# Kernel optimization log

Hardware: AMD Instinct MI355X
Metric: run time of the kernel (lower is better)

Reference implementation:

```python
import jax, jax.numpy as jnp
import numpy as np

B, L, D, E, N, DDELTA, DCONV = 4, 2048, 1024, 2048, 16, 64, 4
EPS = 1e-5


def setup_inputs() -> dict:
    key = jax.random.key(0)
    ks = jax.random.split(key, 12)
    def rn(k, shape, scale=0.02):
        return (jax.random.normal(k, shape) * scale).astype(jnp.float32)
    return {
        "resid":  jax.random.normal(ks[0], (B, L, D), dtype=jnp.float32),
        "norm_w": jnp.ones((D,), jnp.float32),
        "skip_w": rn(ks[1], (E, D)),          # skip_proj.weight
        "in_w":   rn(ks[2], (E, D)),          # in_proj.weight
        "conv_w": rn(ks[3], (E, 1, DCONV), 0.1),  # depthwise conv1d weight
        "conv_b": jnp.zeros((E,), jnp.float32),
        "Wd1":    rn(ks[4], (DDELTA, E)),     # W_delta_1.weight
        "Wd2_w":  rn(ks[5], (E, DDELTA)),     # W_delta_2.weight
        "Wd2_b":  rn(ks[6], (E,), 0.01),      # W_delta_2.bias
        "WB":     rn(ks[7], (N, E)),          # W_B.weight
        "WC":     rn(ks[8], (N, E)),          # W_C.weight
        "A_log":  (jax.random.normal(ks[9], (E, N)) * 0.5).astype(jnp.float32),
        "W_D":    jnp.ones((E,), jnp.float32),
        "out_w":  rn(ks[10], (D, E)),         # out_proj.weight
    }


def reference(resid, norm_w, skip_w, in_w, conv_w, conv_b, Wd1, Wd2_w, Wd2_b,
              WB, WC, A_log, W_D, out_w):
    # RMSNorm
    x = resid * jax.lax.rsqrt(jnp.mean(resid * resid, axis=-1, keepdims=True) + EPS) * norm_w
    skip = x @ skip_w.T                              # [B,L,E]
    x = x @ in_w.T                                   # [B,L,E]
    # depthwise causal conv1d (padding=DCONV-1 then truncate to L == left-pad only)
    xc = jnp.transpose(x, (0, 2, 1))                 # [B,E,L]
    xc = jax.lax.conv_general_dilated(
        xc, conv_w, window_strides=(1,), padding=[(DCONV - 1, 0)],
        dimension_numbers=("NCH", "OIH", "NCH"), feature_group_count=conv_w.shape[0])
    x = jnp.transpose(xc, (0, 2, 1)) + conv_b        # [B,L,E]
    x = jax.nn.silu(x)                               # ssm input

    A = -jnp.exp(A_log)                              # [E,N]
    delta = jax.nn.softplus((x @ Wd1.T) @ Wd2_w.T + Wd2_b)  # [B,L,E]
    Bm = x @ WB.T                                    # [B,L,N]
    Cm = x @ WC.T                                    # [B,L,N]

    def step(h, inp):
        x_l, d_l, B_l, C_l = inp                     # [B,E],[B,E],[B,N],[B,N]
        A_bar = jnp.exp(d_l[:, :, None] * A)         # [B,E,N]
        h = A_bar * h + (d_l * x_l)[:, :, None] * B_l[:, None, :]
        y_l = jnp.einsum("ben,bn->be", h, C_l)       # h @ C
        return h, y_l

    h0 = jnp.zeros((resid.shape[0], A.shape[0], A.shape[1]), x.dtype)
    xs = (jnp.swapaxes(x, 0, 1), jnp.swapaxes(delta, 0, 1),
          jnp.swapaxes(Bm, 0, 1), jnp.swapaxes(Cm, 0, 1))
    _, ys = jax.lax.scan(step, h0, xs)               # ys: [L,B,E]
    y = jnp.swapaxes(ys, 0, 1)                       # [B,L,E]

    y = y + x * W_D
    y = y * jax.nn.silu(skip)
    y = y @ out_w.T                                  # [B,L,D]
    return resid + y
```

## Files before the change

kernel.cpp:

```cpp
#include <hip/hip_runtime.h>
#include <hip/hip_bf16.h>
#include <math.h>

#define B_ 4
#define L_ 2048
#define D_ 1024
#define E_ 2048
#define N_ 16
#define DD_ 64
#define DCONV_ 4

#define S_SEG 8
#define SEGLEN_ (L_ / S_SEG)
#define CL_ 32

typedef __attribute__((ext_vector_type(8))) short bf16x8;
typedef __attribute__((ext_vector_type(4))) float f32x4;

static __device__ __forceinline__ float silu_f(float x) {
    return x / (1.f + __expf(-x));
}

static __device__ __forceinline__ ushort f2bf(float f) {
    __hip_bfloat16 h = __float2bfloat16(f);
    return *reinterpret_cast<ushort*>(&h);
}

__global__ __launch_bounds__(256) void k_rmsnorm_bf(const float* __restrict__ resid,
                                                    const float* __restrict__ nw,
                                                    ushort* __restrict__ out) {
    int row = blockIdx.x;
    const float* r = resid + (size_t)row * D_;
    int t = threadIdx.x;
    float4 v = *reinterpret_cast<const float4*>(&r[t * 4]);
    float ss = v.x * v.x + v.y * v.y + v.z * v.z + v.w * v.w;
#pragma unroll
    for (int o = 32; o >= 1; o >>= 1) ss += __shfl_xor(ss, o, 64);
    __shared__ float red[4];
    if ((t & 63) == 0) red[t >> 6] = ss;
    __syncthreads();
    float tot = red[0] + red[1] + red[2] + red[3];
    float rs = rsqrtf(tot * (1.f / (float)D_) + 1e-5f);
    float4 w4 = *reinterpret_cast<const float4*>(&nw[t * 4]);
    ushort4 o4;
    o4.x = f2bf(v.x * rs * w4.x);
    o4.y = f2bf(v.y * rs * w4.y);
    o4.z = f2bf(v.z * rs * w4.z);
    o4.w = f2bf(v.w * rs * w4.w);
    *reinterpret_cast<ushort4*>(&out[(size_t)row * D_ + t * 4]) = o4;
}

__global__ __launch_bounds__(256) void k_cast_bf(const float* __restrict__ in,
                                                 ushort* __restrict__ out) {
    int i = blockIdx.x * 256 + threadIdx.x;
    float4 v = *reinterpret_cast<const float4*>(&in[i * 4]);
    ushort4 o;
    o.x = f2bf(v.x); o.y = f2bf(v.y); o.z = f2bf(v.z); o.w = f2bf(v.w);
    *reinterpret_cast<ushort4*>(&out[i * 4]) = o;
}

template <int EPI>
__global__ __launch_bounds__(256) void k_gemm_bf(const ushort* __restrict__ A,
                                                 const ushort* __restrict__ W,
                                                 const float* __restrict__ addsrc,
                                                 float* __restrict__ C,
                                                 int M, int N, int K) {
    constexpr int BM = 128, BN = 128, BK = 32, LDB = 40;
    __shared__ __align__(16) ushort As[BM * LDB];
    __shared__ __align__(16) ushort Ws[BN * LDB];
    int t = threadIdx.x;
    int m0 = blockIdx.y * BM, n0 = blockIdx.x * BN;
    int wave = t >> 6, lane = t & 63;
    int wr = wave >> 1, wc = wave & 1;
    int lr = lane & 15, lg = lane >> 4;

    f32x4 acc[4][4] = {};

    for (int k0 = 0; k0 < K; k0 += BK) {
#pragma unroll
        for (int p = 0; p < 2; ++p) {
            int f = t + p * 256;
            int row = f >> 2;
            int cg = (f & 3) * 8;
            *reinterpret_cast<uint4*>(&As[row * LDB + cg]) =
                *reinterpret_cast<const uint4*>(&A[(size_t)(m0 + row) * K + k0 + cg]);
            *reinterpret_cast<uint4*>(&Ws[row * LDB + cg]) =
                *reinterpret_cast<const uint4*>(&W[(size_t)(n0 + row) * K + k0 + cg]);
        }
        __syncthreads();
        bf16x8 af[4], bfr[4];
#pragma unroll
        for (int i = 0; i < 4; ++i) {
            af[i]  = *reinterpret_cast<const bf16x8*>(&As[(wr * 64 + i * 16 + lr) * LDB + lg * 8]);
            bfr[i] = *reinterpret_cast<const bf16x8*>(&Ws[(wc * 64 + i * 16 + lr) * LDB + lg * 8]);
        }
#pragma unroll
        for (int i = 0; i < 4; ++i)
#pragma unroll
            for (int j = 0; j < 4; ++j)
                acc[i][j] = __builtin_amdgcn_mfma_f32_16x16x32_bf16(af[i], bfr[j], acc[i][j], 0, 0, 0);
        __syncthreads();
    }

#pragma unroll
    for (int i = 0; i < 4; ++i) {
        int mrow = m0 + wr * 64 + i * 16 + lg * 4;
#pragma unroll
        for (int j = 0; j < 4; ++j) {
            int ncol = n0 + wc * 64 + j * 16 + lr;
#pragma unroll
            for (int q = 0; q < 4; ++q) {
                float v = acc[i][j][q];
                size_t idx = (size_t)(mrow + q) * N + ncol;
                if (EPI == 2) v += addsrc[idx];
                C[idx] = v;
            }
        }
    }
}

__global__ __launch_bounds__(256) void k_proj(const ushort* __restrict__ A,
                                              const ushort* __restrict__ Wc,
                                              float* __restrict__ Bm,
                                              float* __restrict__ Cm,
                                              float* __restrict__ d1) {
    constexpr int BK = 32, LDB = 40;
    __shared__ __align__(16) ushort As[32 * LDB];
    __shared__ __align__(16) ushort Ws[96 * LDB];
    int t = threadIdx.x;
    int m0 = blockIdx.x * 32;
    int wave = t >> 6, lane = t & 63;
    int rowbase = (wave >> 1) * 16;
    int colbase = (wave & 1) * 48;
    int lr = lane & 15, lg = lane >> 4;

    f32x4 acc[3] = {};

    for (int k0 = 0; k0 < E_; k0 += BK) {
        if (t < 128) {
            int row = t >> 2;
            int cg = (t & 3) * 8;
            *reinterpret_cast<uint4*>(&As[row * LDB + cg]) =
                *reinterpret_cast<const uint4*>(&A[(size_t)(m0 + row) * E_ + k0 + cg]);
        }
        {
            int f = t;
            int row = f >> 2, cg = (f & 3) * 8;
            *reinterpret_cast<uint4*>(&Ws[row * LDB + cg]) =
                *reinterpret_cast<const uint4*>(&Wc[(size_t)row * E_ + k0 + cg]);
            if (t < 128) {
                int f2 = t + 256;
                int row2 = f2 >> 2, cg2 = (f2 & 3) * 8;
                *reinterpret_cast<uint4*>(&Ws[row2 * LDB + cg2]) =
                    *reinterpret_cast<const uint4*>(&Wc[(size_t)row2 * E_ + k0 + cg2]);
            }
        }
        __syncthreads();
        bf16x8 af = *reinterpret_cast<const bf16x8*>(&As[(rowbase + lr) * LDB + lg * 8]);
#pragma unroll
        for (int j = 0; j < 3; ++j) {
            bf16x8 bf = *reinterpret_cast<const bf16x8*>(&Ws[(colbase + j * 16 + lr) * LDB + lg * 8]);
            acc[j] = __builtin_amdgcn_mfma_f32_16x16x32_bf16(af, bf, acc[j], 0, 0, 0);
        }
        __syncthreads();
    }

#pragma unroll
    for (int j = 0; j < 3; ++j) {
        int ncol = colbase + j * 16 + lr;
#pragma unroll
        for (int q = 0; q < 4; ++q) {
            int m = m0 + rowbase + lg * 4 + q;
            float v = acc[j][q];
            if (ncol < 16)      Bm[(size_t)m * 16 + ncol] = v;
            else if (ncol < 32) Cm[(size_t)m * 16 + (ncol - 16)] = v;
            else                d1[(size_t)m * 64 + (ncol - 32)] = v;
        }
    }
}

template <int EPI>
__global__ __launch_bounds__(256) void k_gemm_tn(const float* __restrict__ A,
                                                 const float* __restrict__ W,
                                                 const float* __restrict__ bias,
                                                 float* __restrict__ C,
                                                 int M, int N, int K) {
    constexpr int BM = 64, BN = 64, BK = 32;
    constexpr int LDP = 68;
    __shared__ __align__(16) float As[BK][LDP];
    __shared__ __align__(16) float Ws[BK][LDP];
    int tid = threadIdx.x;
    int tx = tid & 15;
    int ty = tid >> 4;
    int m0 = blockIdx.y * BM;
    int n0 = blockIdx.x * BN;

    float acc[4][4];
#pragma unroll
    for (int i = 0; i < 4; ++i)
#pragma unroll
        for (int j = 0; j < 4; ++j) acc[i][j] = 0.f;

    for (int k0 = 0; k0 < K; k0 += BK) {
#pragma unroll
        for (int p = 0; p < 2; ++p) {
            int idx = tid + p * 256;
            int row = idx >> 3;
            int col4 = (idx & 7) * 4;
            float4 av = *reinterpret_cast<const float4*>(&A[(size_t)(m0 + row) * K + k0 + col4]);
            As[col4 + 0][row] = av.x;
            As[col4 + 1][row] = av.y;
            As[col4 + 2][row] = av.z;
            As[col4 + 3][row] = av.w;
            float4 wv = *reinterpret_cast<const float4*>(&W[(size_t)(n0 + row) * K + k0 + col4]);
            Ws[col4 + 0][row] = wv.x;
            Ws[col4 + 1][row] = wv.y;
            Ws[col4 + 2][row] = wv.z;
            Ws[col4 + 3][row] = wv.w;
        }
        __syncthreads();
#pragma unroll
        for (int kk = 0; kk < BK; ++kk) {
            float4 a4 = *reinterpret_cast<const float4*>(&As[kk][ty * 4]);
            float4 b4 = *reinterpret_cast<const float4*>(&Ws[kk][tx * 4]);
            float a[4] = {a4.x, a4.y, a4.z, a4.w};
            float b[4] = {b4.x, b4.y, b4.z, b4.w};
#pragma unroll
            for (int i = 0; i < 4; ++i)
#pragma unroll
                for (int j = 0; j < 4; ++j) acc[i][j] = fmaf(a[i], b[j], acc[i][j]);
        }
        __syncthreads();
    }

#pragma unroll
    for (int i = 0; i < 4; ++i) {
        int m = m0 + ty * 4 + i;
        int nbase = n0 + tx * 4;
        float4 o4;
        float vals[4];
#pragma unroll
        for (int j = 0; j < 4; ++j) {
            float v = acc[i][j];
            if (EPI == 1) {
                float z = v + bias[nbase + j];
                vals[j] = (z > 20.f) ? z : log1pf(expf(z));
            } else {
                vals[j] = v;
            }
        }
        o4.x = vals[0]; o4.y = vals[1]; o4.z = vals[2]; o4.w = vals[3];
        *reinterpret_cast<float4*>(&C[(size_t)m * N + nbase]) = o4;
    }
}

__global__ __launch_bounds__(256) void k_conv_silu(const float* __restrict__ x,
                                                   const float* __restrict__ w,
                                                   const float* __restrict__ bias,
                                                   float* __restrict__ out,
                                                   ushort* __restrict__ out_bf) {
    int idx = blockIdx.x * 256 + threadIdx.x;
    int e = idx & (E_ - 1);
    int l = (idx / E_) & (L_ - 1);
    float4 wv = *reinterpret_cast<const float4*>(&w[e * 4]);
    float acc = bias[e];
    acc = fmaf(wv.w, x[idx], acc);
    if (l >= 1) acc = fmaf(wv.z, x[idx - E_], acc);
    if (l >= 2) acc = fmaf(wv.y, x[idx - 2 * E_], acc);
    if (l >= 3) acc = fmaf(wv.x, x[idx - 3 * E_], acc);
    float s = silu_f(acc);
    out[idx] = s;
    out_bf[idx] = f2bf(s);
}

__global__ __launch_bounds__(256) void k_scan_p1(const float* __restrict__ xs,
                                                 const float* __restrict__ delta,
                                                 const float* __restrict__ Bm,
                                                 const float* __restrict__ A_log,
                                                 float* __restrict__ hloc,
                                                 float* __restrict__ sdsum) {
    __shared__ __align__(16) float sd[CL_][64];
    __shared__ __align__(16) float sx[CL_][64];
    __shared__ __align__(16) float sB[CL_][16];
    int t = threadIdx.x;
    int q = t & 3, ci = t >> 2;
    int bid = blockIdx.x;
    int s = bid & 7;
    int eblk = (bid >> 3) & 31;
    int b = bid >> 8;
    int e0 = eblk * 64;
    int e = e0 + ci;

    f32x4 A4;
    {
        f32x4 al = *reinterpret_cast<const f32x4*>(&A_log[e * 16 + q * 4]);
#pragma unroll
        for (int i = 0; i < 4; ++i) A4[i] = -__expf(al[i]);
    }
    f32x4 h = {0.f, 0.f, 0.f, 0.f};
    float sdl = 0.f;

    for (int l0 = 0; l0 < SEGLEN_; l0 += CL_) {
        size_t rowbase = (size_t)b * L_ + s * SEGLEN_ + l0;
#pragma unroll
        for (int p = 0; p < 2; ++p) {
            int f = t + p * 256;
            int l = f >> 4;
            int c4 = (f & 15) * 4;
            size_t g = (rowbase + l) * E_ + e0 + c4;
            *reinterpret_cast<f32x4*>(&sd[l][c4]) = *reinterpret_cast<const f32x4*>(&delta[g]);
            *reinterpret_cast<f32x4*>(&sx[l][c4]) = *reinterpret_cast<const f32x4*>(&xs[g]);
        }
        if (t < 128) {
            int l = t >> 2;
            int c4 = (t & 3) * 4;
            *reinterpret_cast<f32x4*>(&sB[l][c4]) =
                *reinterpret_cast<const f32x4*>(&Bm[(rowbase + l) * 16 + c4]);
        }
        __syncthreads();
#pragma unroll 4
        for (int l = 0; l < CL_; ++l) {
            float d = sd[l][ci];
            float xv = sx[l][ci];
            f32x4 Bv = *reinterpret_cast<const f32x4*>(&sB[l][q * 4]);
            f32x4 e4;
#pragma unroll
            for (int i = 0; i < 4; ++i) e4[i] = __expf(d * A4[i]);
            float dx = d * xv;
            h = e4 * h + dx * Bv;
            sdl += d;
        }
        __syncthreads();
    }
    size_t idx = (size_t)(b * S_SEG + s) * E_ + e;
    *reinterpret_cast<f32x4*>(&hloc[idx * 16 + q * 4]) = h;
    if (q == 0) sdsum[idx] = sdl;
}

__global__ __launch_bounds__(256) void k_scan_p2(const float* __restrict__ hloc,
                                                 const float* __restrict__ sdsum,
                                                 const float* __restrict__ A_log,
                                                 float* __restrict__ hin) {
    int t = blockIdx.x * 256 + threadIdx.x;
    int q = t & 3;
    int e = (t >> 2) & (E_ - 1);
    int b = t >> 13;
    f32x4 A4;
    {
        f32x4 al = *reinterpret_cast<const f32x4*>(&A_log[e * 16 + q * 4]);
#pragma unroll
        for (int i = 0; i < 4; ++i) A4[i] = -__expf(al[i]);
    }
    f32x4 acc = {0.f, 0.f, 0.f, 0.f};
#pragma unroll
    for (int s = 0; s < S_SEG; ++s) {
        size_t idx = (size_t)(b * S_SEG + s) * E_ + e;
        *reinterpret_cast<f32x4*>(&hin[idx * 16 + q * 4]) = acc;
        float sd = sdsum[idx];
        f32x4 hl = *reinterpret_cast<const f32x4*>(&hloc[idx * 16 + q * 4]);
        f32x4 p;
#pragma unroll
        for (int i = 0; i < 4; ++i) p[i] = __expf(A4[i] * sd);
        acc = hl + p * acc;
    }
}

__global__ __launch_bounds__(256) void k_scan_p3(const float* __restrict__ xs,
                                                 const float* __restrict__ delta,
                                                 const float* __restrict__ Bm,
                                                 const float* __restrict__ Cm,
                                                 const float* __restrict__ A_log,
                                                 const float* __restrict__ W_D,
                                                 const float* __restrict__ skip,
                                                 const float* __restrict__ hin,
                                                 ushort* __restrict__ yg) {
    __shared__ __align__(16) float sd[CL_][64];
    __shared__ __align__(16) float sx[CL_][64];
    __shared__ __align__(16) float ssk[CL_][64];
    __shared__ __align__(16) float sB[CL_][16];
    __shared__ __align__(16) float sC[CL_][16];
    __shared__ __align__(16) ushort syg[CL_][64];
    int t = threadIdx.x;
    int q = t & 3, ci = t >> 2;
    int bid = blockIdx.x;
    int s = bid & 7;
    int eblk = (bid >> 3) & 31;
    int b = bid >> 8;
    int e0 = eblk * 64;
    int e = e0 + ci;

    f32x4 A4;
    {
        f32x4 al = *reinterpret_cast<const f32x4*>(&A_log[e * 16 + q * 4]);
#pragma unroll
        for (int i = 0; i < 4; ++i) A4[i] = -__expf(al[i]);
    }
    size_t cidx = (size_t)(b * S_SEG + s) * E_ + e;
    f32x4 h = *reinterpret_cast<const f32x4*>(&hin[cidx * 16 + q * 4]);
    float wd = W_D[e];

    for (int l0 = 0; l0 < SEGLEN_; l0 += CL_) {
        size_t rowbase = (size_t)b * L_ + s * SEGLEN_ + l0;
#pragma unroll
        for (int p = 0; p < 2; ++p) {
            int f = t + p * 256;
            int l = f >> 4;
            int c4 = (f & 15) * 4;
            size_t g = (rowbase + l) * E_ + e0 + c4;
            *reinterpret_cast<f32x4*>(&sd[l][c4])  = *reinterpret_cast<const f32x4*>(&delta[g]);
            *reinterpret_cast<f32x4*>(&sx[l][c4])  = *reinterpret_cast<const f32x4*>(&xs[g]);
            *reinterpret_cast<f32x4*>(&ssk[l][c4]) = *reinterpret_cast<const f32x4*>(&skip[g]);
        }
        {
            int f = t & 127;
            int l = f >> 2;
            int c4 = (f & 3) * 4;
            size_t gb = (rowbase + l) * 16 + c4;
            if (t < 128)
                *reinterpret_cast<f32x4*>(&sB[l][c4]) = *reinterpret_cast<const f32x4*>(&Bm[gb]);
            else
                *reinterpret_cast<f32x4*>(&sC[l][c4]) = *reinterpret_cast<const f32x4*>(&Cm[gb]);
        }
        __syncthreads();
#pragma unroll 4
        for (int l = 0; l < CL_; ++l) {
            float d = sd[l][ci];
            float xv = sx[l][ci];
            f32x4 Bv = *reinterpret_cast<const f32x4*>(&sB[l][q * 4]);
            f32x4 Cv = *reinterpret_cast<const f32x4*>(&sC[l][q * 4]);
            f32x4 e4;
#pragma unroll
            for (int i = 0; i < 4; ++i) e4[i] = __expf(d * A4[i]);
            float dx = d * xv;
            h = e4 * h + dx * Bv;
            f32x4 yp = h * Cv;
            float y = (yp[0] + yp[1]) + (yp[2] + yp[3]);
            y += __shfl_xor(y, 1, 64);
            y += __shfl_xor(y, 2, 64);
            if (q == 0) {
                float g = silu_f(ssk[l][ci]);
                syg[l][ci] = f2bf((y + xv * wd) * g);
            }
        }
        __syncthreads();
        {
            int l = t >> 3;
            int col = (t & 7) * 8;
            *reinterpret_cast<uint4*>(&yg[(rowbase + l) * E_ + e0 + col]) =
                *reinterpret_cast<const uint4*>(&syg[l][col]);
        }
    }
}

extern "C" void kernel_launch(void* const* d_in, const int* in_sizes, int n_in,
                              void* d_out, int out_size, void* d_ws, size_t ws_size,
                              hipStream_t stream) {
    const float* resid  = (const float*)d_in[0];
    const float* norm_w = (const float*)d_in[1];
    const float* skip_w = (const float*)d_in[2];
    const float* in_w   = (const float*)d_in[3];
    const float* conv_w = (const float*)d_in[4];
    const float* conv_b = (const float*)d_in[5];
    const float* Wd1    = (const float*)d_in[6];
    const float* Wd2_w  = (const float*)d_in[7];
    const float* Wd2_b  = (const float*)d_in[8];
    const float* WB     = (const float*)d_in[9];
    const float* WC     = (const float*)d_in[10];
    const float* A_log  = (const float*)d_in[11];
    const float* W_D    = (const float*)d_in[12];
    const float* out_w  = (const float*)d_in[13];
    float* out = (float*)d_out;

    const int M = B_ * L_;
    char* p = (char*)d_ws;
    ushort* xn_bf   = (ushort*)p;  p += (size_t)M * D_ * 2;
    ushort* skw_bf  = (ushort*)p;  p += (size_t)E_ * D_ * 2;
    ushort* inw_bf  = (ushort*)p;  p += (size_t)E_ * D_ * 2;
    ushort* outw_bf = (ushort*)p;  p += (size_t)D_ * E_ * 2;
    ushort* yg_bf   = (ushort*)p;  p += (size_t)M * E_ * 2;
    float*  skipb   = (float*)p;   p += (size_t)M * E_ * 4;
    float*  xin     = (float*)p;   p += (size_t)M * E_ * 4;
    float*  xs      = (float*)p;   p += (size_t)M * E_ * 4;
    float*  d1      = (float*)p;   p += (size_t)M * DD_ * 4;
    float*  Bm      = (float*)p;   p += (size_t)M * 16 * 4;
    float*  Cm      = (float*)p;   p += (size_t)M * 16 * 4;
    ushort* wbc_bf  = (ushort*)p;  p += (size_t)96 * E_ * 2;
    float*  delta   = xin;
    ushort* xs_bf   = yg_bf;
    float*  hloc    = (float*)xn_bf;
    float*  hin     = hloc + (size_t)B_ * S_SEG * E_ * 16;
    float*  sdsum   = hin  + (size_t)B_ * S_SEG * E_ * 16;

    dim3 blk(256);

    k_cast_bf<<<dim3((E_ * D_) / 1024), blk, 0, stream>>>(skip_w, skw_bf);
    k_cast_bf<<<dim3((E_ * D_) / 1024), blk, 0, stream>>>(in_w, inw_bf);
    k_cast_bf<<<dim3((D_ * E_) / 1024), blk, 0, stream>>>(out_w, outw_bf);
    k_cast_bf<<<dim3((N_ * E_) / 1024), blk, 0, stream>>>(WB, wbc_bf);
    k_cast_bf<<<dim3((N_ * E_) / 1024), blk, 0, stream>>>(WC, wbc_bf + (size_t)16 * E_);
    k_cast_bf<<<dim3((DD_ * E_) / 1024), blk, 0, stream>>>(Wd1, wbc_bf + (size_t)32 * E_);
    k_rmsnorm_bf<<<dim3(M), blk, 0, stream>>>(resid, norm_w, xn_bf);
    k_gemm_bf<0><<<dim3(E_ / 128, M / 128), blk, 0, stream>>>(xn_bf, skw_bf, nullptr, skipb, M, E_, D_);
    k_gemm_bf<0><<<dim3(E_ / 128, M / 128), blk, 0, stream>>>(xn_bf, inw_bf, nullptr, xin, M, E_, D_);
    k_conv_silu<<<dim3((M * E_) / 256), blk, 0, stream>>>(xin, conv_w, conv_b, xs, xs_bf);
    k_proj<<<dim3(M / 32), blk, 0, stream>>>(xs_bf, wbc_bf, Bm, Cm, d1);
    k_gemm_tn<1><<<dim3(E_ / 64, M / 64), blk, 0, stream>>>(d1, Wd2_w, Wd2_b, delta, M, E_, DD_);
    k_scan_p1<<<dim3(B_ * 32 * S_SEG), blk, 0, stream>>>(xs, delta, Bm, A_log, hloc, sdsum);
    k_scan_p2<<<dim3((B_ * E_ * 4) / 256), blk, 0, stream>>>(hloc, sdsum, A_log, hin);
    k_scan_p3<<<dim3(B_ * 32 * S_SEG), blk, 0, stream>>>(xs, delta, Bm, Cm, A_log, W_D,
                                                          skipb, hin, yg_bf);
    k_gemm_bf<2><<<dim3(D_ / 128, M / 128), blk, 0, stream>>>(yg_bf, outw_bf, resid, out, M, D_, E_);
}
```

Before: 664.9 us.

## Restructure scan to one-thread-per-channel, async LDS GEMM loads, bf16 MFMA delta projection

The chunked scan drops its LDS staging and 4-thread-per-channel layout. Each thread now owns one channel with all 16 states in registers, across 32 segments instead of 8, and uses exp2f with pre-scaled A. The bf16 GEMM loads tiles with global_load_lds direct-to-LDS into an unpadded layout. The fp32 SIMT delta GEMM is replaced by the bf16 MFMA GEMM with a fused softplus epilogue, and d1 is now stored as bf16. Risks include LDS bank conflicts from removing the padding, reduced precision in delta, and more register pressure in the scan.

```diff
diff --git a/kernel.cpp b/kernel.cpp
--- a/kernel.cpp
+++ b/kernel.cpp
@@ -10,12 +10,14 @@
 #define DD_ 64
 #define DCONV_ 4
 
-#define S_SEG 8
+#define S_SEG 32
 #define SEGLEN_ (L_ / S_SEG)
-#define CL_ 32
 
 typedef __attribute__((ext_vector_type(8))) short bf16x8;
 typedef __attribute__((ext_vector_type(4))) float f32x4;
+
+typedef __attribute__((address_space(1))) const void gvoid_t;
+typedef __attribute__((address_space(3))) void lvoid_t;
 
 static __device__ __forceinline__ float silu_f(float x) {
     return x / (1.f + __expf(-x));
@@ -25,6 +27,8 @@
     __hip_bfloat16 h = __float2bfloat16(f);
     return *reinterpret_cast<ushort*>(&h);
 }
+
+#define LOG2E_ 1.4426950408889634f
 
 __global__ __launch_bounds__(256) void k_rmsnorm_bf(const float* __restrict__ resid,
                                                     const float* __restrict__ nw,
@@ -62,37 +66,41 @@
 template <int EPI>
 __global__ __launch_bounds__(256) void k_gemm_bf(const ushort* __restrict__ A,
                                                  const ushort* __restrict__ W,
+                                                 const float* __restrict__ bias,
                                                  const float* __restrict__ addsrc,
                                                  float* __restrict__ C,
                                                  int M, int N, int K) {
-    constexpr int BM = 128, BN = 128, BK = 32, LDB = 40;
-    __shared__ __align__(16) ushort As[BM * LDB];
-    __shared__ __align__(16) ushort Ws[BN * LDB];
+    constexpr int BM = 128, BN = 128, BK = 32;
+    __shared__ __align__(16) ushort As[BM * BK];
+    __shared__ __align__(16) ushort Ws[BN * BK];
     int t = threadIdx.x;
     int m0 = blockIdx.y * BM, n0 = blockIdx.x * BN;
     int wave = t >> 6, lane = t & 63;
     int wr = wave >> 1, wc = wave & 1;
     int lr = lane & 15, lg = lane >> 4;
+    int srow = lane >> 2;
+    int scol = (lane & 3) * 8;
 
     f32x4 acc[4][4] = {};
 
     for (int k0 = 0; k0 < K; k0 += BK) {
 #pragma unroll
         for (int p = 0; p < 2; ++p) {
-            int f = t + p * 256;
-            int row = f >> 2;
-            int cg = (f & 3) * 8;
-            *reinterpret_cast<uint4*>(&As[row * LDB + cg]) =
-                *reinterpret_cast<const uint4*>(&A[(size_t)(m0 + row) * K + k0 + cg]);
-            *reinterpret_cast<uint4*>(&Ws[row * LDB + cg]) =
-                *reinterpret_cast<const uint4*>(&W[(size_t)(n0 + row) * K + k0 + cg]);
+            int seg = wave * 2 + p;
+            int row = seg * 16 + srow;
+            __builtin_amdgcn_global_load_lds(
+                (gvoid_t*)(A + (size_t)(m0 + row) * K + k0 + scol),
+                (lvoid_t*)(As + seg * 512), 16, 0, 0);
+            __builtin_amdgcn_global_load_lds(
+                (gvoid_t*)(W + (size_t)(n0 + row) * K + k0 + scol),
+                (lvoid_t*)(Ws + seg * 512), 16, 0, 0);
         }
         __syncthreads();
         bf16x8 af[4], bfr[4];
 #pragma unroll
         for (int i = 0; i < 4; ++i) {
-            af[i]  = *reinterpret_cast<const bf16x8*>(&As[(wr * 64 + i * 16 + lr) * LDB + lg * 8]);
-            bfr[i] = *reinterpret_cast<const bf16x8*>(&Ws[(wc * 64 + i * 16 + lr) * LDB + lg * 8]);
+            af[i]  = *reinterpret_cast<const bf16x8*>(&As[(wr * 64 + i * 16 + lr) * BK + lg * 8]);
+            bfr[i] = *reinterpret_cast<const bf16x8*>(&Ws[(wc * 64 + i * 16 + lr) * BK + lg * 8]);
         }
 #pragma unroll
         for (int i = 0; i < 4; ++i)
@@ -112,6 +120,10 @@
             for (int q = 0; q < 4; ++q) {
                 float v = acc[i][j][q];
                 size_t idx = (size_t)(mrow + q) * N + ncol;
+                if (EPI == 1) {
+                    float z = v + bias[ncol];
+                    v = (z > 20.f) ? z : log1pf(expf(z));
+                }
                 if (EPI == 2) v += addsrc[idx];
                 C[idx] = v;
             }
@@ -123,7 +135,7 @@
                                               const ushort* __restrict__ Wc,
                                               float* __restrict__ Bm,
                                               float* __restrict__ Cm,
-                                              float* __restrict__ d1) {
+                                              ushort* __restrict__ d1_bf) {
     constexpr int BK = 32, LDB = 40;
     __shared__ __align__(16) ushort As[32 * LDB];
     __shared__ __align__(16) ushort Ws[96 * LDB];
@@ -174,83 +186,8 @@
             float v = acc[j][q];
             if (ncol < 16)      Bm[(size_t)m * 16 + ncol] = v;
             else if (ncol < 32) Cm[(size_t)m * 16 + (ncol - 16)] = v;
-            else                d1[(size_t)m * 64 + (ncol - 32)] = v;
-        }
-    }
-}
-
-template <int EPI>
-__global__ __launch_bounds__(256) void k_gemm_tn(const float* __restrict__ A,
-                                                 const float* __restrict__ W,
-                                                 const float* __restrict__ bias,
-                                                 float* __restrict__ C,
-                                                 int M, int N, int K) {
-    constexpr int BM = 64, BN = 64, BK = 32;
-    constexpr int LDP = 68;
-    __shared__ __align__(16) float As[BK][LDP];
-    __shared__ __align__(16) float Ws[BK][LDP];
-    int tid = threadIdx.x;
-    int tx = tid & 15;
-    int ty = tid >> 4;
-    int m0 = blockIdx.y * BM;
-    int n0 = blockIdx.x * BN;
-
-    float acc[4][4];
-#pragma unroll
-    for (int i = 0; i < 4; ++i)
-#pragma unroll
-        for (int j = 0; j < 4; ++j) acc[i][j] = 0.f;
-
-    for (int k0 = 0; k0 < K; k0 += BK) {
-#pragma unroll
-        for (int p = 0; p < 2; ++p) {
-            int idx = tid + p * 256;
-            int row = idx >> 3;
-            int col4 = (idx & 7) * 4;
-            float4 av = *reinterpret_cast<const float4*>(&A[(size_t)(m0 + row) * K + k0 + col4]);
-            As[col4 + 0][row] = av.x;
-            As[col4 + 1][row] = av.y;
-            As[col4 + 2][row] = av.z;
-            As[col4 + 3][row] = av.w;
-            float4 wv = *reinterpret_cast<const float4*>(&W[(size_t)(n0 + row) * K + k0 + col4]);
-            Ws[col4 + 0][row] = wv.x;
-            Ws[col4 + 1][row] = wv.y;
-            Ws[col4 + 2][row] = wv.z;
-            Ws[col4 + 3][row] = wv.w;
-        }
-        __syncthreads();
-#pragma unroll
-        for (int kk = 0; kk < BK; ++kk) {
-            float4 a4 = *reinterpret_cast<const float4*>(&As[kk][ty * 4]);
-            float4 b4 = *reinterpret_cast<const float4*>(&Ws[kk][tx * 4]);
-            float a[4] = {a4.x, a4.y, a4.z, a4.w};
-            float b[4] = {b4.x, b4.y, b4.z, b4.w};
-#pragma unroll
-            for (int i = 0; i < 4; ++i)
-#pragma unroll
-                for (int j = 0; j < 4; ++j) acc[i][j] = fmaf(a[i], b[j], acc[i][j]);
-        }
-        __syncthreads();
-    }
-
-#pragma unroll
-    for (int i = 0; i < 4; ++i) {
-        int m = m0 + ty * 4 + i;
-        int nbase = n0 + tx * 4;
-        float4 o4;
-        float vals[4];
-#pragma unroll
-        for (int j = 0; j < 4; ++j) {
-            float v = acc[i][j];
-            if (EPI == 1) {
-                float z = v + bias[nbase + j];
-                vals[j] = (z > 20.f) ? z : log1pf(expf(z));
-            } else {
-                vals[j] = v;
-            }
-        }
-        o4.x = vals[0]; o4.y = vals[1]; o4.z = vals[2]; o4.w = vals[3];
-        *reinterpret_cast<float4*>(&C[(size_t)m * N + nbase]) = o4;
+            else                d1_bf[(size_t)m * 64 + (ncol - 32)] = f2bf(v);
+        }
     }
 }
 
@@ -273,94 +210,81 @@
     out_bf[idx] = f2bf(s);
 }
 
+
 __global__ __launch_bounds__(256) void k_scan_p1(const float* __restrict__ xs,
                                                  const float* __restrict__ delta,
                                                  const float* __restrict__ Bm,
                                                  const float* __restrict__ A_log,
-                                                 float* __restrict__ hloc,
+                                                 float* __restrict__ hbuf,
                                                  float* __restrict__ sdsum) {
-    __shared__ __align__(16) float sd[CL_][64];
-    __shared__ __align__(16) float sx[CL_][64];
-    __shared__ __align__(16) float sB[CL_][16];
     int t = threadIdx.x;
-    int q = t & 3, ci = t >> 2;
     int bid = blockIdx.x;
-    int s = bid & 7;
-    int eblk = (bid >> 3) & 31;
+    int s = bid & (S_SEG - 1);
+    int eblk = (bid >> 5) & 7;
     int b = bid >> 8;
-    int e0 = eblk * 64;
-    int e = e0 + ci;
-
-    f32x4 A4;
-    {
-        f32x4 al = *reinterpret_cast<const f32x4*>(&A_log[e * 16 + q * 4]);
-#pragma unroll
-        for (int i = 0; i < 4; ++i) A4[i] = -__expf(al[i]);
-    }
-    f32x4 h = {0.f, 0.f, 0.f, 0.f};
+    int e = eblk * 256 + t;
+
+    float A2[16];
+#pragma unroll
+    for (int i = 0; i < 16; i += 4) {
+        f32x4 al = *reinterpret_cast<const f32x4*>(&A_log[(size_t)e * 16 + i]);
+#pragma unroll
+        for (int j = 0; j < 4; ++j) A2[i + j] = -__expf(al[j]) * LOG2E_;
+    }
+    f32x4 h4[4] = {};
     float sdl = 0.f;
 
-    for (int l0 = 0; l0 < SEGLEN_; l0 += CL_) {
-        size_t rowbase = (size_t)b * L_ + s * SEGLEN_ + l0;
-#pragma unroll
-        for (int p = 0; p < 2; ++p) {
-            int f = t + p * 256;
-            int l = f >> 4;
-            int c4 = (f & 15) * 4;
-            size_t g = (rowbase + l) * E_ + e0 + c4;
-            *reinterpret_cast<f32x4*>(&sd[l][c4]) = *reinterpret_cast<const f32x4*>(&delta[g]);
-            *reinterpret_cast<f32x4*>(&sx[l][c4]) = *reinterpret_cast<const f32x4*>(&xs[g]);
-        }
-        if (t < 128) {
-            int l = t >> 2;
-            int c4 = (t & 3) * 4;
-            *reinterpret_cast<f32x4*>(&sB[l][c4]) =
-                *reinterpret_cast<const f32x4*>(&Bm[(rowbase + l) * 16 + c4]);
-        }
-        __syncthreads();
-#pragma unroll 4
-        for (int l = 0; l < CL_; ++l) {
-            float d = sd[l][ci];
-            float xv = sx[l][ci];
-            f32x4 Bv = *reinterpret_cast<const f32x4*>(&sB[l][q * 4]);
+    const float* dp = delta + ((size_t)b * L_ + s * SEGLEN_) * E_ + e;
+    const float* xp = xs    + ((size_t)b * L_ + s * SEGLEN_) * E_ + e;
+    const float* Bp = Bm + ((size_t)b * L_ + s * SEGLEN_) * 16;
+
+#pragma unroll 2
+    for (int l = 0; l < SEGLEN_; ++l) {
+        float d  = dp[(size_t)l * E_];
+        float xv = xp[(size_t)l * E_];
+        f32x4 B4[4];
+#pragma unroll
+        for (int g = 0; g < 4; ++g)
+            B4[g] = *reinterpret_cast<const f32x4*>(&Bp[l * 16 + g * 4]);
+        float dx = d * xv;
+        sdl += d;
+#pragma unroll
+        for (int g = 0; g < 4; ++g) {
             f32x4 e4;
 #pragma unroll
-            for (int i = 0; i < 4; ++i) e4[i] = __expf(d * A4[i]);
-            float dx = d * xv;
-            h = e4 * h + dx * Bv;
-            sdl += d;
-        }
-        __syncthreads();
-    }
-    size_t idx = (size_t)(b * S_SEG + s) * E_ + e;
-    *reinterpret_cast<f32x4*>(&hloc[idx * 16 + q * 4]) = h;
-    if (q == 0) sdsum[idx] = sdl;
-}
-
-__global__ __launch_bounds__(256) void k_scan_p2(const float* __restrict__ hloc,
+            for (int j = 0; j < 4; ++j) e4[j] = exp2f(d * A2[g * 4 + j]);
+            h4[g] = e4 * h4[g] + dx * B4[g];
+        }
+    }
+    size_t cidx = ((size_t)(b * S_SEG + s) * E_ + e) * 16;
+#pragma unroll
+    for (int g = 0; g < 4; ++g)
+        *reinterpret_cast<f32x4*>(&hbuf[cidx + g * 4]) = h4[g];
+    sdsum[(size_t)(b * S_SEG + s) * E_ + e] = sdl;
+}
+
+__global__ __launch_bounds__(256) void k_scan_p2(float* __restrict__ hbuf,
                                                  const float* __restrict__ sdsum,
-                                                 const float* __restrict__ A_log,
-                                                 float* __restrict__ hin) {
+                                                 const float* __restrict__ A_log) {
     int t = blockIdx.x * 256 + threadIdx.x;
     int q = t & 3;
     int e = (t >> 2) & (E_ - 1);
     int b = t >> 13;
-    f32x4 A4;
+    f32x4 A2;
     {
-        f32x4 al = *reinterpret_cast<const f32x4*>(&A_log[e * 16 + q * 4]);
-#pragma unroll
-        for (int i = 0; i < 4; ++i) A4[i] = -__expf(al[i]);
+        f32x4 al = *reinterpret_cast<const f32x4*>(&A_log[(size_t)e * 16 + q * 4]);
+#pragma unroll
+        for (int i = 0; i < 4; ++i) A2[i] = -__expf(al[i]) * LOG2E_;
     }
     f32x4 acc = {0.f, 0.f, 0.f, 0.f};
-#pragma unroll
     for (int s = 0; s < S_SEG; ++s) {
-        size_t idx = (size_t)(b * S_SEG + s) * E_ + e;
-        *reinterpret_cast<f32x4*>(&hin[idx * 16 + q * 4]) = acc;
-        float sd = sdsum[idx];
-        f32x4 hl = *reinterpret_cast<const f32x4*>(&hloc[idx * 16 + q * 4]);
+        size_t idx = ((size_t)(b * S_SEG + s) * E_ + e) * 16 + q * 4;
+        f32x4 hl = *reinterpret_cast<const f32x4*>(&hbuf[idx]);
+        float sd = sdsum[(size_t)(b * S_SEG + s) * E_ + e];
+        *reinterpret_cast<f32x4*>(&hbuf[idx]) = acc;
         f32x4 p;
 #pragma unroll
-        for (int i = 0; i < 4; ++i) p[i] = __expf(A4[i] * sd);
+        for (int i = 0; i < 4; ++i) p[i] = exp2f(A2[i] * sd);
         acc = hl + p * acc;
     }
 }
@@ -372,83 +296,60 @@
                                                  const float* __restrict__ A_log,
                                                  const float* __restrict__ W_D,
                                                  const float* __restrict__ skip,
-                                                 const float* __restrict__ hin,
+                                                 const float* __restrict__ hbuf,
                                                  ushort* __restrict__ yg) {
-    __shared__ __align__(16) float sd[CL_][64];
-    __shared__ __align__(16) float sx[CL_][64];
-    __shared__ __align__(16) float ssk[CL_][64];
-    __shared__ __align__(16) float sB[CL_][16];
-    __shared__ __align__(16) float sC[CL_][16];
-    __shared__ __align__(16) ushort syg[CL_][64];
     int t = threadIdx.x;
-    int q = t & 3, ci = t >> 2;
     int bid = blockIdx.x;
-    int s = bid & 7;
-    int eblk = (bid >> 3) & 31;
+    int s = bid & (S_SEG - 1);
+    int eblk = (bid >> 5) & 7;
     int b = bid >> 8;
-    int e0 = eblk * 64;
-    int e = e0 + ci;
-
-    f32x4 A4;
-    {
-        f32x4 al = *reinterpret_cast<const f32x4*>(&A_log[e * 16 + q * 4]);
-#pragma unroll
-        for (int i = 0; i < 4; ++i) A4[i] = -__expf(al[i]);
-    }
-    size_t cidx = (size_t)(b * S_SEG + s) * E_ + e;
-    f32x4 h = *reinterpret_cast<const f32x4*>(&hin[cidx * 16 + q * 4]);
+    int e = eblk * 256 + t;
+
+    float A2[16];
+#pragma unroll
+    for (int i = 0; i < 16; i += 4) {
+        f32x4 al = *reinterpret_cast<const f32x4*>(&A_log[(size_t)e * 16 + i]);
+#pragma unroll
+        for (int j = 0; j < 4; ++j) A2[i + j] = -__expf(al[j]) * LOG2E_;
+    }
+    size_t cidx = ((size_t)(b * S_SEG + s) * E_ + e) * 16;
+    f32x4 h4[4];
+#pragma unroll
+    for (int g = 0; g < 4; ++g)
+        h4[g] = *reinterpret_cast<const f32x4*>(&hbuf[cidx + g * 4]);
     float wd = W_D[e];
 
-    for (int l0 = 0; l0 < SEGLEN_; l0 += CL_) {
-        size_t rowbase = (size_t)b * L_ + s * SEGLEN_ + l0;
-#pragma unroll
-        for (int p = 0; p < 2; ++p) {
-            int f = t + p * 256;
-            int l = f >> 4;
-            int c4 = (f & 15) * 4;
-            size_t g = (rowbase + l) * E_ + e0 + c4;
-            *reinterpret_cast<f32x4*>(&sd[l][c4])  = *reinterpret_cast<const f32x4*>(&delta[g]);
-            *reinterpret_cast<f32x4*>(&sx[l][c4])  = *reinterpret_cast<const f32x4*>(&xs[g]);
-            *reinterpret_cast<f32x4*>(&ssk[l][c4]) = *reinterpret_cast<const f32x4*>(&skip[g]);
-        }
-        {
-            int f = t & 127;
-            int l = f >> 2;
-            int c4 = (f & 3) * 4;
-            size_t gb = (rowbase + l) * 16 + c4;
-            if (t < 128)
-                *reinterpret_cast<f32x4*>(&sB[l][c4]) = *reinterpret_cast<const f32x4*>(&Bm[gb]);
-            else
-                *reinterpret_cast<f32x4*>(&sC[l][c4]) = *reinterpret_cast<const f32x4*>(&Cm[gb]);
-        }
-        __syncthreads();
-#pragma unroll 4
-        for (int l = 0; l < CL_; ++l) {
-            float d = sd[l][ci];
-            float xv = sx[l][ci];
-            f32x4 Bv = *reinterpret_cast<const f32x4*>(&sB[l][q * 4]);
-            f32x4 Cv = *reinterpret_cast<const f32x4*>(&sC[l][q * 4]);
+    const float* dp = delta + ((size_t)b * L_ + s * SEGLEN_) * E_ + e;
+    const float* xp = xs    + ((size_t)b * L_ + s * SEGLEN_) * E_ + e;
+    const float* sp = skip  + ((size_t)b * L_ + s * SEGLEN_) * E_ + e;
+    const float* Bp = Bm + ((size_t)b * L_ + s * SEGLEN_) * 16;
+    const float* Cp = Cm + ((size_t)b * L_ + s * SEGLEN_) * 16;
+    ushort* yp = yg + ((size_t)b * L_ + s * SEGLEN_) * E_ + e;
+
+#pragma unroll 2
+    for (int l = 0; l < SEGLEN_; ++l) {
+        float d  = dp[(size_t)l * E_];
+        float xv = xp[(size_t)l * E_];
+        float sk = sp[(size_t)l * E_];
+        f32x4 B4[4], C4[4];
+#pragma unroll
+        for (int g = 0; g < 4; ++g) {
+            B4[g] = *reinterpret_cast<const f32x4*>(&Bp[l * 16 + g * 4]);
+            C4[g] = *reinterpret_cast<const f32x4*>(&Cp[l * 16 + g * 4]);
+        }
+        float dx = d * xv;
+        f32x4 yv = {0.f, 0.f, 0.f, 0.f};
+#pragma unroll
+        for (int g = 0; g < 4; ++g) {
             f32x4 e4;
 #pragma unroll
-            for (int i = 0; i < 4; ++i) e4[i] = __expf(d * A4[i]);
-            float dx = d * xv;
-            h = e4 * h + dx * Bv;
-            f32x4 yp = h * Cv;
-            float y = (yp[0] + yp[1]) + (yp[2] + yp[3]);
-            y += __shfl_xor(y, 1, 64);
-            y += __shfl_xor(y, 2, 64);
-            if (q == 0) {
-                float g = silu_f(ssk[l][ci]);
-                syg[l][ci] = f2bf((y + xv * wd) * g);
-            }
-        }
-        __syncthreads();
-        {
-            int l = t >> 3;
-            int col = (t & 7) * 8;
-            *reinterpret_cast<uint4*>(&yg[(rowbase + l) * E_ + e0 + col]) =
-                *reinterpret_cast<const uint4*>(&syg[l][col]);
-        }
+            for (int j = 0; j < 4; ++j) e4[j] = exp2f(d * A2[g * 4 + j]);
+            h4[g] = e4 * h4[g] + dx * B4[g];
+            yv = h4[g] * C4[g] + yv;
+        }
+        float y = (yv[0] + yv[1]) + (yv[2] + yv[3]);
+        float gsk = silu_f(sk);
+        yp[(size_t)l * E_] = f2bf((y + xv * wd) * gsk);
     }
 }
 
@@ -481,15 +382,15 @@
     float*  skipb   = (float*)p;   p += (size_t)M * E_ * 4;
     float*  xin     = (float*)p;   p += (size_t)M * E_ * 4;
     float*  xs      = (float*)p;   p += (size_t)M * E_ * 4;
-    float*  d1      = (float*)p;   p += (size_t)M * DD_ * 4;
+    ushort* d1_bf   = (ushort*)p;  p += (size_t)M * DD_ * 2;
     float*  Bm      = (float*)p;   p += (size_t)M * 16 * 4;
     float*  Cm      = (float*)p;   p += (size_t)M * 16 * 4;
     ushort* wbc_bf  = (ushort*)p;  p += (size_t)96 * E_ * 2;
+    ushort* wd2_bf  = (ushort*)p;  p += (size_t)E_ * DD_ * 2;
     float*  delta   = xin;
     ushort* xs_bf   = yg_bf;
-    float*  hloc    = (float*)xn_bf;
-    float*  hin     = hloc + (size_t)B_ * S_SEG * E_ * 16;
-    float*  sdsum   = hin  + (size_t)B_ * S_SEG * E_ * 16;
+    float*  hbuf    = (float*)xn_bf;
+    float*  sdsum   = hbuf + (size_t)B_ * S_SEG * E_ * 16;
 
     dim3 blk(256);
 
@@ -499,15 +400,16 @@
     k_cast_bf<<<dim3((N_ * E_) / 1024), blk, 0, stream>>>(WB, wbc_bf);
     k_cast_bf<<<dim3((N_ * E_) / 1024), blk, 0, stream>>>(WC, wbc_bf + (size_t)16 * E_);
     k_cast_bf<<<dim3((DD_ * E_) / 1024), blk, 0, stream>>>(Wd1, wbc_bf + (size_t)32 * E_);
+    k_cast_bf<<<dim3((E_ * DD_) / 1024), blk, 0, stream>>>(Wd2_w, wd2_bf);
     k_rmsnorm_bf<<<dim3(M), blk, 0, stream>>>(resid, norm_w, xn_bf);
-    k_gemm_bf<0><<<dim3(E_ / 128, M / 128), blk, 0, stream>>>(xn_bf, skw_bf, nullptr, skipb, M, E_, D_);
-    k_gemm_bf<0><<<dim3(E_ / 128, M / 128), blk, 0, stream>>>(xn_bf, inw_bf, nullptr, xin, M, E_, D_);
+    k_gemm_bf<0><<<dim3(E_ / 128, M / 128), blk, 0, stream>>>(xn_bf, skw_bf, nullptr, nullptr, skipb, M, E_, D_);
+    k_gemm_bf<0><<<dim3(E_ / 128, M / 128), blk, 0, stream>>>(xn_bf, inw_bf, nullptr, nullptr, xin, M, E_, D_);
     k_conv_silu<<<dim3((M * E_) / 256), blk, 0, stream>>>(xin, conv_w, conv_b, xs, xs_bf);
-    k_proj<<<dim3(M / 32), blk, 0, stream>>>(xs_bf, wbc_bf, Bm, Cm, d1);
-    k_gemm_tn<1><<<dim3(E_ / 64, M / 64), blk, 0, stream>>>(d1, Wd2_w, Wd2_b, delta, M, E_, DD_);
-    k_scan_p1<<<dim3(B_ * 32 * S_SEG), blk, 0, stream>>>(xs, delta, Bm, A_log, hloc, sdsum);
-    k_scan_p2<<<dim3((B_ * E_ * 4) / 256), blk, 0, stream>>>(hloc, sdsum, A_log, hin);
-    k_scan_p3<<<dim3(B_ * 32 * S_SEG), blk, 0, stream>>>(xs, delta, Bm, Cm, A_log, W_D,
-                                                          skipb, hin, yg_bf);
-    k_gemm_bf<2><<<dim3(D_ / 128, M / 128), blk, 0, stream>>>(yg_bf, outw_bf, resid, out, M, D_, E_);
-}
+    k_proj<<<dim3(M / 32), blk, 0, stream>>>(xs_bf, wbc_bf, Bm, Cm, d1_bf);
+    k_gemm_bf<1><<<dim3(E_ / 128, M / 128), blk, 0, stream>>>(d1_bf, wd2_bf, Wd2_b, nullptr, delta, M, E_, DD_);
+    k_scan_p1<<<dim3(B_ * S_SEG * (E_ / 256)), blk, 0, stream>>>(xs, delta, Bm, A_log, hbuf, sdsum);
+    k_scan_p2<<<dim3((B_ * E_ * 4) / 256), blk, 0, stream>>>(hbuf, sdsum, A_log);
+    k_scan_p3<<<dim3(B_ * S_SEG * (E_ / 256)), blk, 0, stream>>>(xs, delta, Bm, Cm, A_log, W_D,
+                                                                  skipb, hbuf, yg_bf);
+    k_gemm_bf<2><<<dim3(D_ / 128, M / 128), blk, 0, stream>>>(yg_bf, outw_bf, nullptr, resid, out, M, D_, E_);
+}
```

New measurement: 666.3 us. No clear change (+0.2%).
